# Kernel optimization log

Hardware: AMD Instinct MI355X
Metric: run time of the kernel (lower is better)

Reference implementation:

```python
import jax, jax.numpy as jnp
import numpy as np

W = 32        # local_context
M = 128       # nb_features
TEMP = 1.0    # softmax_temp
NEG = -1e24   # mask fill used by local_dot_product in the original


def _log_features(x, proj):
    # Performer softmax-kernel log-features (before stabilization).
    # x: (B,H,N,E), proj: (M,E) -> (B,H,N,M); exp(q.k*TEMP) ~ (1/M) sum_m phi_q phi_k
    xn = x * np.float32(np.sqrt(TEMP))
    d = jnp.einsum('bhne,me->bhnm', xn, proj)
    diag = 0.5 * jnp.sum(xn * xn, axis=-1, keepdims=True)
    return d - diag


def _sb_local_chunk(q, k, v, proj):
    # Scatterbrain SBLocalAttention: exact softmax scores inside a centered local
    # window of size W, Performer low-rank approximation outside, shared normalizer.
    # q: (B,H,L,E) chunk queries; k,v: (B,H,S,E); proj: (M,E)
    B, H, L, E = q.shape
    S = k.shape[2]
    nb, half = L // W, W // 2

    logq = _log_features(q, proj)
    stab_q = jax.lax.stop_gradient(jnp.max(logq, axis=-1, keepdims=True))        # per-query stabilizer
    phi_q = jnp.exp(logq - stab_q)
    logk = _log_features(k, proj)
    stab_k = jax.lax.stop_gradient(jnp.max(logk, axis=(-1, -2), keepdims=True))  # global key stabilizer
    phi_k = jnp.exp(logk - stab_k)
    # true low-rank score = (phi_q . phi_k) * exp(prime_log_scale)
    pls = stab_q[..., 0] + stab_k[..., 0] - np.float32(np.log(M))                # (B,H,L)

    # Low-rank (linear attention) sums over ALL keys
    kv = jnp.einsum('bhsm,bhsd->bhmd', phi_k, v)
    lr_v = jnp.einsum('bhlm,bhmd->bhld', phi_q, kv)            # (B,H,L,E)
    lr_1 = jnp.einsum('bhlm,bhm->bhl', phi_q, phi_k.sum(2))    # (B,H,L)

    # Local window: query position t attends keys [t-W//2, t+W//2).
    # Gather 3 key blocks of size W per query block instead of per-query windows.
    q_blk = q.reshape(B, H, nb, W, E)
    phiq_blk = phi_q.reshape(B, H, nb, W, M)
    idx3 = W * jnp.arange(nb)[:, None] + jnp.arange(3 * W)[None, :]   # (nb,3W) into padded seq
    pad = [(0, 0), (0, 0), (W, W), (0, 0)]
    k3 = jnp.pad(k, pad)[:, :, idx3]          # (B,H,nb,3W,E)
    v3 = jnp.pad(v, pad)[:, :, idx3]
    phik3 = jnp.pad(phi_k, pad)[:, :, idx3]   # (B,H,nb,3W,M)

    pos = idx3[:, None, :] - W                # absolute key positions (nb,1,3W)
    rel = pos - (W * jnp.arange(nb)[:, None, None] + jnp.arange(W)[None, :, None])
    mask = (rel >= -half) & (rel < half) & (pos >= 0) & (pos < S)     # (nb,W,3W)

    scores = TEMP * jnp.einsum('bhnqe,bhnke->bhnqk', q_blk, k3)
    scores = jnp.where(mask, scores, NEG)
    dots_p = jnp.where(mask, jnp.einsum('bhnqm,bhnkm->bhnqk', phiq_blk, phik3), 0.0)

    qk_lse = jax.nn.logsumexp(scores, axis=-1).reshape(B, H, L)
    # low-rank mass minus the in-window part it double counts (>= 0 since phi >= 0)
    lr_rem = jnp.clip(lr_1 - dots_p.sum(-1).reshape(B, H, L), 1e-24, None)
    log_norm = jnp.logaddexp(qk_lse, jnp.log(lr_rem) + pls)           # (B,H,L)

    p_local = jnp.exp(scores - log_norm.reshape(B, H, nb, W, 1))
    out_local = jnp.einsum('bhnqk,bhnke->bhnqe', p_local, v3).reshape(B, H, L, E)
    lr_v_win = jnp.einsum('bhnqk,bhnke->bhnqe', dots_p, v3).reshape(B, H, L, E)
    return out_local + (lr_v - lr_v_win) * jnp.exp(pls - log_norm)[..., None]


def _forward(query, key, value, proj):
    # query/key/value: (B,T,H,E) as in the torch module; proj: (4,M,E), one random
    # feature matrix per chunk (module builds a fresh SBLocalAttention each chunk).
    q = jnp.transpose(query, (0, 2, 1, 3))
    k = jnp.transpose(key, (0, 2, 1, 3))
    v = jnp.transpose(value, (0, 2, 1, 3))
    B, H, T, E = q.shape
    CH = 1024
    qc = q.reshape(B, H, T // CH, CH, E).transpose(2, 0, 1, 3, 4)     # (4,B,H,CH,E)
    outs = jax.vmap(_sb_local_chunk, in_axes=(0, None, None, 0))(qc, k, v, proj)
    # torch.cat(att, 1).transpose(1, 2) -> (B,H,T,E)
    return outs.transpose(1, 2, 0, 3, 4).reshape(B, H, T, E)


def setup_inputs() -> dict:
    key = jax.random.key(0)
    k1, k2, k3, k4 = jax.random.split(key, 4)
    B, T, S, H, E = 4, 4096, 4096, 8, 64
    return {
        'query': jax.random.normal(k1, (B, T, H, E), dtype=jnp.float32),
        'key': jax.random.normal(k2, (B, S, H, E), dtype=jnp.float32),
        'value': jax.random.normal(k3, (B, S, H, E), dtype=jnp.float32),
        'proj': jax.random.normal(k4, (4, M, E), dtype=jnp.float32),
    }


def reference(query, key, value, proj):
    return _forward(query, key, value, proj)
```

## Files before the change

kernel.cpp:

```cpp
#include <hip/hip_runtime.h>

typedef unsigned short u16;
typedef unsigned int   u32;
typedef __attribute__((ext_vector_type(8))) short short8;
typedef __attribute__((ext_vector_type(4))) float f32x4;

#define LOGM 4.852030263919617f

constexpr int WS_PMAX = 0;
constexpr int WS_K1   = 2048;
constexpr int WS_KV   = 18432;
constexpr int WS_PHIK = 1067008;

__device__ __forceinline__ float b2f(u16 u){ union { u32 i; float f; } x; x.i = ((u32)u) << 16; return x.f; }
__device__ __forceinline__ u16 f2b(float f){ union { float f; u32 i; } x; x.f = f; return (u16)((x.i + 0x7fffu + ((x.i >> 16) & 1u)) >> 16); }

__global__ __launch_bounds__(128) void k_stab(const float* __restrict__ proj,
                                              float* __restrict__ ws){
  __shared__ float red[2];
  const int c = blockIdx.x, tid = threadIdx.x;
  const int wave = tid >> 6, l = tid & 63;
  const float4* pr = (const float4*)(proj + c*8192 + tid*64);
  float pn = 0.f;
  #pragma unroll
  for(int i=0;i<16;i++){ float4 u = pr[i]; pn = fmaf(u.x,u.x,fmaf(u.y,u.y,fmaf(u.z,u.z,fmaf(u.w,u.w,pn)))); }
  #pragma unroll
  for(int o=1;o<64;o<<=1) pn = fmaxf(pn, __shfl_xor(pn, o));
  if(l == 0) red[wave] = pn;
  __syncthreads();
  const float stab = 0.5f * fmaxf(red[0], red[1]);
  if(tid < 32) ws[WS_PMAX + c*32 + tid] = stab;
}

__global__ __launch_bounds__(256, 2) void k_phi(const float* __restrict__ key,
                                                const float* __restrict__ val,
                                                const float* __restrict__ proj,
                                                float* __restrict__ ws){
  __shared__ __align__(16) u16 phit[128*72];
  __shared__ __align__(16) u16 vt[64*72];
  const int tid = threadIdx.x;
  const int wave = tid >> 6, l = tid & 63;
  const int g = l >> 4, r16 = l & 15;
  const int kq = blockIdx.x, combo = blockIdx.y;
  const int c = combo >> 5, b = (combo >> 3) & 3, h = combo & 7;
  const float* projc = proj + c*8192;
  const float stab = ws[WS_PMAX + combo];

  short8 ph[8][2], pl[8][2];
  #pragma unroll
  for(int mt=0;mt<8;mt++){
    #pragma unroll
    for(int ks=0;ks<2;ks++){
      const float* pb = projc + (mt*16 + r16)*64 + ks*32 + g*8;
      float4 u0 = *(const float4*)pb;
      float4 u1 = *(const float4*)(pb + 4);
      float x[8] = {u0.x,u0.y,u0.z,u0.w,u1.x,u1.y,u1.z,u1.w};
      #pragma unroll
      for(int j=0;j<8;j++){
        u16 hb = f2b(x[j]);
        ph[mt][ks][j] = (short)hb;
        pl[mt][ks][j] = (short)f2b(x[j] - b2f(hb));
      }
    }
  }

  const f32x4 zero4 = {0.f,0.f,0.f,0.f};
  f32x4 kvacc[2][4];
  #pragma unroll
  for(int i=0;i<2;i++)
    #pragma unroll
    for(int j=0;j<4;j++) kvacc[i][j] = zero4;
  float k1p0 = 0.f, k1p1 = 0.f;
  u16* phikg = ((u16*)(ws + WS_PHIK)) + (size_t)combo*1056*128;

  for(int t0=0;t0<16;t0++){
    const int s_tile = (kq + 4*t0)*64;
    const bool dtile = (s_tile < 1056);
    const int sA = s_tile + wave*16 + r16;
    const float* krow = key + (size_t)(b*4096 + sA)*512 + h*64;
    float areg[16];
    #pragma unroll
    for(int ks=0;ks<2;ks++){
      float4 u0 = *(const float4*)(krow + ks*32 + g*8);
      float4 u1 = *(const float4*)(krow + ks*32 + g*8 + 4);
      areg[ks*8+0]=u0.x; areg[ks*8+1]=u0.y; areg[ks*8+2]=u0.z; areg[ks*8+3]=u0.w;
      areg[ks*8+4]=u1.x; areg[ks*8+5]=u1.y; areg[ks*8+6]=u1.z; areg[ks*8+7]=u1.w;
    }
    float4 vreg[4];
    #pragma unroll
    for(int i=0;i<4;i++){
      int flat = tid + 256*i;
      int sv = flat >> 4, d4 = (flat & 15)*4;
      vreg[i] = *(const float4*)(val + (size_t)(b*4096 + s_tile + sv)*512 + h*64 + d4);
    }
    float ksq = 0.f;
    #pragma unroll
    for(int e=0;e<16;e++) ksq = fmaf(areg[e], areg[e], ksq);
    ksq += __shfl_xor(ksq, 16);
    ksq += __shfl_xor(ksq, 32);
    ksq *= 0.5f;
    short8 ah[2], al[2];
    #pragma unroll
    for(int ks=0;ks<2;ks++){
      #pragma unroll
      for(int j=0;j<8;j++){
        float x = areg[ks*8+j];
        u16 hb = f2b(x);
        ah[ks][j] = (short)hb;
        al[ks][j] = (short)f2b(x - b2f(hb));
      }
    }
    f32x4 acc[8];
    #pragma unroll
    for(int mt=0;mt<8;mt++) acc[mt] = zero4;
    #pragma unroll
    for(int ks=0;ks<2;ks++){
      #pragma unroll
      for(int mt=0;mt<8;mt++){
        acc[mt] = __builtin_amdgcn_mfma_f32_16x16x32_bf16(ah[ks], ph[mt][ks], acc[mt], 0, 0, 0);
        acc[mt] = __builtin_amdgcn_mfma_f32_16x16x32_bf16(ah[ks], pl[mt][ks], acc[mt], 0, 0, 0);
        acc[mt] = __builtin_amdgcn_mfma_f32_16x16x32_bf16(al[ks], ph[mt][ks], acc[mt], 0, 0, 0);
      }
    }
    const float kc0 = __shfl(ksq, 4*g + 0);
    const float kc1 = __shfl(ksq, 4*g + 1);
    const float kc2 = __shfl(ksq, 4*g + 2);
    const float kc3 = __shfl(ksq, 4*g + 3);
    const int gs = s_tile + wave*16 + r16;
    #pragma unroll
    for(int mt=0;mt<8;mt++){
      ushort4 pw;
      pw.x = f2b(__expf(acc[mt][0] - kc0 - stab));
      pw.y = f2b(__expf(acc[mt][1] - kc1 - stab));
      pw.z = f2b(__expf(acc[mt][2] - kc2 - stab));
      pw.w = f2b(__expf(acc[mt][3] - kc3 - stab));
      *(ushort4*)(phit + (mt*16 + r16)*72 + wave*16 + 4*g) = pw;
      if(dtile && gs < 1056)
        *(ushort4*)(phikg + (size_t)gs*128 + mt*16 + 4*g) = pw;
    }
    #pragma unroll
    for(int i=0;i<4;i++){
      int flat = tid + 256*i;
      int sv = flat >> 4, d4 = (flat & 15)*4;
      float x[4] = {vreg[i].x, vreg[i].y, vreg[i].z, vreg[i].w};
      #pragma unroll
      for(int j=0;j<4;j++){
        int d = d4 + j;
        vt[d*72 + (sv ^ (8*((d>>2)&7)))] = f2b(x[j]);
      }
    }
    __syncthreads();
    #pragma unroll
    for(int ks=0;ks<2;ks++){
      short8 af0 = *(const short8*)(phit + ((2*wave+0)*16 + r16)*72 + ks*32 + g*8);
      short8 af1 = *(const short8*)(phit + ((2*wave+1)*16 + r16)*72 + ks*32 + g*8);
      short8 bf[4];
      #pragma unroll
      for(int dt=0;dt<4;dt++){
        int d = dt*16 + r16;
        int col = (ks*32 + g*8) ^ (8*((d>>2)&7));
        bf[dt] = *(const short8*)(vt + d*72 + col);
      }
      #pragma unroll
      for(int dt=0;dt<4;dt++){
        kvacc[0][dt] = __builtin_amdgcn_mfma_f32_16x16x32_bf16(af0, bf[dt], kvacc[0][dt], 0, 0, 0);
        kvacc[1][dt] = __builtin_amdgcn_mfma_f32_16x16x32_bf16(af1, bf[dt], kvacc[1][dt], 0, 0, 0);
      }
      #pragma unroll
      for(int j=0;j<8;j++){ k1p0 += b2f((u16)af0[j]); k1p1 += b2f((u16)af1[j]); }
    }
    __syncthreads();
  }
  k1p0 += __shfl_xor(k1p0, 16); k1p0 += __shfl_xor(k1p0, 32);
  k1p1 += __shfl_xor(k1p1, 16); k1p1 += __shfl_xor(k1p1, 32);
  if(l < 16){
    atomicAdd(ws + WS_K1 + combo*128 + (2*wave+0)*16 + l, k1p0);
    atomicAdd(ws + WS_K1 + combo*128 + (2*wave+1)*16 + l, k1p1);
  }
  #pragma unroll
  for(int mi=0;mi<2;mi++){
    #pragma unroll
    for(int dt=0;dt<4;dt++){
      #pragma unroll
      for(int rr=0;rr<4;rr++){
        int m = (2*wave+mi)*16 + 4*g + rr;
        int d = dt*16 + r16;
        atomicAdd(ws + WS_KV + (size_t)combo*8192 + m*64 + d, kvacc[mi][dt][rr]);
      }
    }
  }
}

__global__ __launch_bounds__(256, 2) void k_qm(const float* __restrict__ qry,
                                               const float* __restrict__ key,
                                               const float* __restrict__ val,
                                               const float* __restrict__ proj,
                                               float* __restrict__ ws,
                                               float* __restrict__ out){
  __shared__ __align__(16) u16 buf[30720];
  u16* kvtA   = buf;
  u16* phiqsA = buf + 8704;
  float* k1s  = (float*)(buf + 17408);
  u16* khs  = buf;
  u16* kls  = buf + 6912;
  u16* phik = buf + 13824;
  u16* cjh  = buf;
  u16* cjl  = buf + 8704;
  u16* vt   = buf + 17408;
  u16* vtl  = buf + 24064;

  const int tid = threadIdx.x;
  const int wave = tid >> 6, l = tid & 63;
  const int g = l >> 4, r16 = l & 15;
  const int qt = blockIdx.x, combo = blockIdx.y;
  const int c = combo >> 5, b = (combo >> 3) & 3, h = combo & 7;
  const int s_base = qt*64 - 16;
  const float* projc = proj + c*8192;
  const float stab = ws[WS_PMAX + combo];
  const f32x4 zero4 = {0.f,0.f,0.f,0.f};

  if(tid < 128) k1s[tid] = ws[WS_K1 + combo*128 + tid];
  const float* kvg = ws + WS_KV + (size_t)combo*8192;
  #pragma unroll
  for(int i=0;i<8;i++){
    int flat = tid + 256*i;
    int m = flat >> 4, d4 = (flat & 15)*4;
    float4 u = *(const float4*)(kvg + m*64 + d4);
    kvtA[(d4+0)*136 + m] = f2b(u.x);
    kvtA[(d4+1)*136 + m] = f2b(u.y);
    kvtA[(d4+2)*136 + m] = f2b(u.z);
    kvtA[(d4+3)*136 + m] = f2b(u.w);
  }
  const int qrow = qt*64 + wave*16 + r16;
  const float* qr = qry + (size_t)(b*4096 + (c*1024 + qrow))*512 + h*64;
  float areg[16];
  #pragma unroll
  for(int ks=0;ks<2;ks++){
    float4 u0 = *(const float4*)(qr + ks*32 + g*8);
    float4 u1 = *(const float4*)(qr + ks*32 + g*8 + 4);
    areg[ks*8+0]=u0.x; areg[ks*8+1]=u0.y; areg[ks*8+2]=u0.z; areg[ks*8+3]=u0.w;
    areg[ks*8+4]=u1.x; areg[ks*8+5]=u1.y; areg[ks*8+6]=u1.z; areg[ks*8+7]=u1.w;
  }
  float qsq = 0.f;
  #pragma unroll
  for(int e=0;e<16;e++) qsq = fmaf(areg[e], areg[e], qsq);
  qsq += __shfl_xor(qsq, 16);
  qsq += __shfl_xor(qsq, 32);
  qsq *= 0.5f;
  short8 ah[2], al[2];
  #pragma unroll
  for(int ks=0;ks<2;ks++){
    #pragma unroll
    for(int j=0;j<8;j++){
      float x = areg[ks*8+j];
      u16 hb = f2b(x);
      ah[ks][j] = (short)hb;
      al[ks][j] = (short)f2b(x - b2f(hb));
    }
  }
  __syncthreads();

  f32x4 acc[8];
  #pragma unroll
  for(int mt=0;mt<8;mt++) acc[mt] = zero4;
  #pragma unroll
  for(int ks=0;ks<2;ks++){
    #pragma unroll
    for(int mt=0;mt<8;mt++){
      const float* pb = projc + (mt*16 + r16)*64 + ks*32 + g*8;
      float4 u0 = *(const float4*)pb;
      float4 u1 = *(const float4*)(pb + 4);
      float x[8] = {u0.x,u0.y,u0.z,u0.w,u1.x,u1.y,u1.z,u1.w};
      short8 pph, ppl;
      #pragma unroll
      for(int j=0;j<8;j++){
        u16 hb = f2b(x[j]);
        pph[j] = (short)hb;
        ppl[j] = (short)f2b(x[j] - b2f(hb));
      }
      acc[mt] = __builtin_amdgcn_mfma_f32_16x16x32_bf16(ah[ks], pph, acc[mt], 0, 0, 0);
      acc[mt] = __builtin_amdgcn_mfma_f32_16x16x32_bf16(ah[ks], ppl, acc[mt], 0, 0, 0);
      acc[mt] = __builtin_amdgcn_mfma_f32_16x16x32_bf16(al[ks], pph, acc[mt], 0, 0, 0);
    }
  }
  float qsr[4];
  #pragma unroll
  for(int r=0;r<4;r++) qsr[r] = __shfl(qsq, 4*g + r);
  float amax[4];
  #pragma unroll
  for(int r=0;r<4;r++){
    float m = -3e38f;
    #pragma unroll
    for(int mt=0;mt<8;mt++) m = fmaxf(m, acc[mt][r]);
    m = fmaxf(m, __shfl_xor(m, 1));
    m = fmaxf(m, __shfl_xor(m, 2));
    m = fmaxf(m, __shfl_xor(m, 4));
    m = fmaxf(m, __shfl_xor(m, 8));
    amax[r] = m;
  }
  float lrp[4] = {0.f,0.f,0.f,0.f};
  #pragma unroll
  for(int mt=0;mt<8;mt++){
    const float k1v = k1s[mt*16 + r16];
    #pragma unroll
    for(int r=0;r<4;r++){
      float phv = __expf(acc[mt][r] - amax[r]);
      phiqsA[(wave*16 + 4*g + r)*136 + mt*16 + r16] = f2b(phv);
      lrp[r] = fmaf(phv, k1v, lrp[r]);
    }
  }
  #pragma unroll
  for(int r=0;r<4;r++){
    lrp[r] += __shfl_xor(lrp[r], 1);
    lrp[r] += __shfl_xor(lrp[r], 2);
    lrp[r] += __shfl_xor(lrp[r], 4);
    lrp[r] += __shfl_xor(lrp[r], 8);
  }
  float plsr[4], lr1r[4];
  #pragma unroll
  for(int r=0;r<4;r++){
    plsr[r] = amax[r] - qsr[r] + stab - LOGM;
    lr1r[r] = lrp[r];
  }
  __syncthreads();

  short8 pa[4];
  #pragma unroll
  for(int ks=0;ks<4;ks++)
    pa[ks] = *(const short8*)(phiqsA + (wave*16 + r16)*136 + ks*32 + g*8);
  f32x4 lacc[4];
  #pragma unroll
  for(int dt=0;dt<4;dt++) lacc[dt] = zero4;
  #pragma unroll
  for(int ks=0;ks<4;ks++){
    #pragma unroll
    for(int dt=0;dt<4;dt++){
      short8 bfr = *(const short8*)(kvtA + (dt*16 + r16)*136 + ks*32 + g*8);
      lacc[dt] = __builtin_amdgcn_mfma_f32_16x16x32_bf16(pa[ks], bfr, lacc[dt], 0, 0, 0);
    }
  }
  __syncthreads();

  const u16* phikg = ((const u16*)(ws + WS_PHIK)) + (size_t)combo*1056*128;
  float4 vreg[6];
  #pragma unroll
  for(int i=0;i<6;i++){
    int flat = tid + 256*i;
    int j = flat >> 4, e4 = (flat & 15)*4;
    int s = s_base + j;
    float4 u = {0.f,0.f,0.f,0.f};
    float4 w4 = {0.f,0.f,0.f,0.f};
    if(s >= 0){
      u  = *(const float4*)(key + (((size_t)b*4096 + s)*8 + h)*64 + e4);
      w4 = *(const float4*)(val + (((size_t)b*4096 + s)*8 + h)*64 + e4);
    }
    vreg[i] = w4;
    ushort4 hh, ll;
    hh.x = f2b(u.x); ll.x = f2b(u.x - b2f(hh.x));
    hh.y = f2b(u.y); ll.y = f2b(u.y - b2f(hh.y));
    hh.z = f2b(u.z); ll.z = f2b(u.z - b2f(hh.z));
    hh.w = f2b(u.w); ll.w = f2b(u.w - b2f(hh.w));
    *(ushort4*)(khs + j*72 + e4) = hh;
    *(ushort4*)(kls + j*72 + e4) = ll;
  }
  #pragma unroll
  for(int i=0;i<12;i++){
    int flat = tid + 256*i;
    int j = flat >> 5, c4 = (flat & 31)*4;
    int s = s_base + j;
    ushort4 p = {0,0,0,0};
    if(s >= 0) p = *(const ushort4*)(phikg + (size_t)s*128 + c4);
    *(ushort4*)(phik + j*136 + c4) = p;
  }
  __syncthreads();

  f32x4 sacc[6], dacc[6];
  #pragma unroll
  for(int j=0;j<6;j++){ sacc[j] = zero4; dacc[j] = zero4; }
  #pragma unroll
  for(int j=0;j<6;j++){
    #pragma unroll
    for(int ks=0;ks<2;ks++){
      short8 kbh = *(const short8*)(khs + (j*16 + r16)*72 + ks*32 + g*8);
      short8 kbl = *(const short8*)(kls + (j*16 + r16)*72 + ks*32 + g*8);
      sacc[j] = __builtin_amdgcn_mfma_f32_16x16x32_bf16(ah[ks], kbh, sacc[j], 0, 0, 0);
      sacc[j] = __builtin_amdgcn_mfma_f32_16x16x32_bf16(al[ks], kbh, sacc[j], 0, 0, 0);
      sacc[j] = __builtin_amdgcn_mfma_f32_16x16x32_bf16(ah[ks], kbl, sacc[j], 0, 0, 0);
    }
    #pragma unroll
    for(int ks=0;ks<4;ks++){
      short8 pb = *(const short8*)(phik + (j*16 + r16)*136 + ks*32 + g*8);
      dacc[j] = __builtin_amdgcn_mfma_f32_16x16x32_bf16(pa[ks], pb, dacc[j], 0, 0, 0);
    }
  }
  __syncthreads();

  #pragma unroll
  for(int i=0;i<6;i++){
    int flat = tid + 256*i;
    int j = flat >> 4, e4 = (flat & 15)*4;
    float4 u = vreg[i];
    u16 h0 = f2b(u.x), h1 = f2b(u.y), h2 = f2b(u.z), h3 = f2b(u.w);
    vt[(e4+0)*104 + j] = h0; vtl[(e4+0)*104 + j] = f2b(u.x - b2f(h0));
    vt[(e4+1)*104 + j] = h1; vtl[(e4+1)*104 + j] = f2b(u.y - b2f(h1));
    vt[(e4+2)*104 + j] = h2; vtl[(e4+2)*104 + j] = f2b(u.z - b2f(h2));
    vt[(e4+3)*104 + j] = h3; vtl[(e4+3)*104 + j] = f2b(u.w - b2f(h3));
  }
  const int rowb = wave*16 + 4*g;
  float m1r[4] = {-1e30f,-1e30f,-1e30f,-1e30f};
  #pragma unroll
  for(int j=0;j<6;j++){
    #pragma unroll
    for(int r=0;r<4;r++){
      int rel = 16*j + r16 - 16 - (rowb + r);
      bool ok = (rel >= -16) && (rel < 16) && (s_base + 16*j + r16 >= 0);
      if(ok) m1r[r] = fmaxf(m1r[r], sacc[j][r]);
    }
  }
  #pragma unroll
  for(int r=0;r<4;r++){
    m1r[r] = fmaxf(m1r[r], __shfl_xor(m1r[r], 1));
    m1r[r] = fmaxf(m1r[r], __shfl_xor(m1r[r], 2));
    m1r[r] = fmaxf(m1r[r], __shfl_xor(m1r[r], 4));
    m1r[r] = fmaxf(m1r[r], __shfl_xor(m1r[r], 8));
  }
  float ser[4] = {0.f,0.f,0.f,0.f}, wpr[4] = {0.f,0.f,0.f,0.f};
  #pragma unroll
  for(int j=0;j<6;j++){
    #pragma unroll
    for(int r=0;r<4;r++){
      int rel = 16*j + r16 - 16 - (rowb + r);
      bool ok = (rel >= -16) && (rel < 16) && (s_base + 16*j + r16 >= 0);
      if(ok){
        ser[r] += __expf(sacc[j][r] - m1r[r]);
        wpr[r] += dacc[j][r];
      }
    }
  }
  #pragma unroll
  for(int r=0;r<4;r++){
    ser[r] += __shfl_xor(ser[r], 1); ser[r] += __shfl_xor(ser[r], 2);
    ser[r] += __shfl_xor(ser[r], 4); ser[r] += __shfl_xor(ser[r], 8);
    wpr[r] += __shfl_xor(wpr[r], 1); wpr[r] += __shfl_xor(wpr[r], 2);
    wpr[r] += __shfl_xor(wpr[r], 4); wpr[r] += __shfl_xor(wpr[r], 8);
  }
  float lnr[4], scr[4];
  #pragma unroll
  for(int r=0;r<4;r++){
    float qk_lse = m1r[r] + __logf(ser[r]);
    float lrem = fmaxf(lr1r[r] - wpr[r], 1e-37f);
    float bb = __logf(lrem) + plsr[r];
    float ln = fmaxf(qk_lse, bb) + log1pf(__expf(-fabsf(qk_lse - bb)));
    lnr[r] = ln;
    scr[r] = __expf(plsr[r] - ln);
  }
  #pragma unroll
  for(int j=0;j<6;j++){
    #pragma unroll
    for(int r=0;r<4;r++){
      int rel = 16*j + r16 - 16 - (rowb + r);
      bool ok = (rel >= -16) && (rel < 16) && (s_base + 16*j + r16 >= 0);
      float cj = ok ? (__expf(sacc[j][r] - lnr[r]) - scr[r]*dacc[j][r]) : 0.f;
      u16 hb = f2b(cj);
      cjh[(rowb + r)*136 + 16*j + r16] = hb;
      cjl[(rowb + r)*136 + 16*j + r16] = f2b(cj - b2f(hb));
    }
  }
  __syncthreads();

  f32x4 oacc[4];
  #pragma unroll
  for(int dt=0;dt<4;dt++) oacc[dt] = zero4;
  #pragma unroll
  for(int ks=0;ks<3;ks++){
    short8 ch = *(const short8*)(cjh + (wave*16 + r16)*136 + ks*32 + g*8);
    short8 cl = *(const short8*)(cjl + (wave*16 + r16)*136 + ks*32 + g*8);
    #pragma unroll
    for(int dt=0;dt<4;dt++){
      short8 vbh = *(const short8*)(vt  + (dt*16 + r16)*104 + ks*32 + g*8);
      short8 vbl = *(const short8*)(vtl + (dt*16 + r16)*104 + ks*32 + g*8);
      oacc[dt] = __builtin_amdgcn_mfma_f32_16x16x32_bf16(ch, vbh, oacc[dt], 0, 0, 0);
      oacc[dt] = __builtin_amdgcn_mfma_f32_16x16x32_bf16(cl, vbh, oacc[dt], 0, 0, 0);
      oacc[dt] = __builtin_amdgcn_mfma_f32_16x16x32_bf16(ch, vbl, oacc[dt], 0, 0, 0);
    }
  }
  #pragma unroll
  for(int r=0;r<4;r++){
    int row = rowb + r;
    float* ob = out + ((((size_t)b*8 + h)*4096) + (size_t)c*1024 + qt*64 + row)*64;
    #pragma unroll
    for(int dt=0;dt<4;dt++)
      ob[dt*16 + r16] = oacc[dt][r] + scr[r]*lacc[dt][r];
  }
}

extern "C" void kernel_launch(void* const* d_in, const int* in_sizes, int n_in,
                              void* d_out, int out_size, void* d_ws, size_t ws_size,
                              hipStream_t stream){
  (void)in_sizes; (void)n_in; (void)out_size; (void)ws_size;
  const float* q = (const float*)d_in[0];
  const float* k = (const float*)d_in[1];
  const float* v = (const float*)d_in[2];
  const float* p = (const float*)d_in[3];
  float* out = (float*)d_out;
  float* ws = (float*)d_ws;
  hipMemsetAsync(ws + WS_K1, 0, (size_t)(16384 + 1048576)*sizeof(float), stream);
  k_stab<<<dim3(4),      128, 0, stream>>>(p, ws);
  k_phi <<<dim3(4,128),  256, 0, stream>>>(k, v, p, ws);
  k_qm  <<<dim3(16,128), 256, 0, stream>>>(q, k, v, p, ws, out);
}
```

Baseline: 324.1 us.

## Prefetch key/value/phi_k tiles early and XOR-swizzle LDS transposed buffers

Moves the global loads of the key, value and phi_k window tiles to the start of the main kernel, holding them in registers so their latency overlaps the query feature and low-rank MFMA phases. It also applies XOR swizzles to the column index of the transposed kv, v and cj shared-memory buffers to reduce LDS bank conflicts on the strided transpose stores. The prefetch adds about 48 live registers per thread, which may lower occupancy or cause spills.

Result: faster. 315.9 us (-2.5%).

```diff
diff --git a/kernel.cpp b/kernel.cpp
--- a/kernel.cpp
+++ b/kernel.cpp
@@ -219,130 +219,9 @@
   const float stab = ws[WS_PMAX + combo];
   const f32x4 zero4 = {0.f,0.f,0.f,0.f};
 
-  if(tid < 128) k1s[tid] = ws[WS_K1 + combo*128 + tid];
-  const float* kvg = ws + WS_KV + (size_t)combo*8192;
-  #pragma unroll
-  for(int i=0;i<8;i++){
-    int flat = tid + 256*i;
-    int m = flat >> 4, d4 = (flat & 15)*4;
-    float4 u = *(const float4*)(kvg + m*64 + d4);
-    kvtA[(d4+0)*136 + m] = f2b(u.x);
-    kvtA[(d4+1)*136 + m] = f2b(u.y);
-    kvtA[(d4+2)*136 + m] = f2b(u.z);
-    kvtA[(d4+3)*136 + m] = f2b(u.w);
-  }
-  const int qrow = qt*64 + wave*16 + r16;
-  const float* qr = qry + (size_t)(b*4096 + (c*1024 + qrow))*512 + h*64;
-  float areg[16];
-  #pragma unroll
-  for(int ks=0;ks<2;ks++){
-    float4 u0 = *(const float4*)(qr + ks*32 + g*8);
-    float4 u1 = *(const float4*)(qr + ks*32 + g*8 + 4);
-    areg[ks*8+0]=u0.x; areg[ks*8+1]=u0.y; areg[ks*8+2]=u0.z; areg[ks*8+3]=u0.w;
-    areg[ks*8+4]=u1.x; areg[ks*8+5]=u1.y; areg[ks*8+6]=u1.z; areg[ks*8+7]=u1.w;
-  }
-  float qsq = 0.f;
-  #pragma unroll
-  for(int e=0;e<16;e++) qsq = fmaf(areg[e], areg[e], qsq);
-  qsq += __shfl_xor(qsq, 16);
-  qsq += __shfl_xor(qsq, 32);
-  qsq *= 0.5f;
-  short8 ah[2], al[2];
-  #pragma unroll
-  for(int ks=0;ks<2;ks++){
-    #pragma unroll
-    for(int j=0;j<8;j++){
-      float x = areg[ks*8+j];
-      u16 hb = f2b(x);
-      ah[ks][j] = (short)hb;
-      al[ks][j] = (short)f2b(x - b2f(hb));
-    }
-  }
-  __syncthreads();
-
-  f32x4 acc[8];
-  #pragma unroll
-  for(int mt=0;mt<8;mt++) acc[mt] = zero4;
-  #pragma unroll
-  for(int ks=0;ks<2;ks++){
-    #pragma unroll
-    for(int mt=0;mt<8;mt++){
-      const float* pb = projc + (mt*16 + r16)*64 + ks*32 + g*8;
-      float4 u0 = *(const float4*)pb;
-      float4 u1 = *(const float4*)(pb + 4);
-      float x[8] = {u0.x,u0.y,u0.z,u0.w,u1.x,u1.y,u1.z,u1.w};
-      short8 pph, ppl;
-      #pragma unroll
-      for(int j=0;j<8;j++){
-        u16 hb = f2b(x[j]);
-        pph[j] = (short)hb;
-        ppl[j] = (short)f2b(x[j] - b2f(hb));
-      }
-      acc[mt] = __builtin_amdgcn_mfma_f32_16x16x32_bf16(ah[ks], pph, acc[mt], 0, 0, 0);
-      acc[mt] = __builtin_amdgcn_mfma_f32_16x16x32_bf16(ah[ks], ppl, acc[mt], 0, 0, 0);
-      acc[mt] = __builtin_amdgcn_mfma_f32_16x16x32_bf16(al[ks], pph, acc[mt], 0, 0, 0);
-    }
-  }
-  float qsr[4];
-  #pragma unroll
-  for(int r=0;r<4;r++) qsr[r] = __shfl(qsq, 4*g + r);
-  float amax[4];
-  #pragma unroll
-  for(int r=0;r<4;r++){
-    float m = -3e38f;
-    #pragma unroll
-    for(int mt=0;mt<8;mt++) m = fmaxf(m, acc[mt][r]);
-    m = fmaxf(m, __shfl_xor(m, 1));
-    m = fmaxf(m, __shfl_xor(m, 2));
-    m = fmaxf(m, __shfl_xor(m, 4));
-    m = fmaxf(m, __shfl_xor(m, 8));
-    amax[r] = m;
-  }
-  float lrp[4] = {0.f,0.f,0.f,0.f};
-  #pragma unroll
-  for(int mt=0;mt<8;mt++){
-    const float k1v = k1s[mt*16 + r16];
-    #pragma unroll
-    for(int r=0;r<4;r++){
-      float phv = __expf(acc[mt][r] - amax[r]);
-      phiqsA[(wave*16 + 4*g + r)*136 + mt*16 + r16] = f2b(phv);
-      lrp[r] = fmaf(phv, k1v, lrp[r]);
-    }
-  }
-  #pragma unroll
-  for(int r=0;r<4;r++){
-    lrp[r] += __shfl_xor(lrp[r], 1);
-    lrp[r] += __shfl_xor(lrp[r], 2);
-    lrp[r] += __shfl_xor(lrp[r], 4);
-    lrp[r] += __shfl_xor(lrp[r], 8);
-  }
-  float plsr[4], lr1r[4];
-  #pragma unroll
-  for(int r=0;r<4;r++){
-    plsr[r] = amax[r] - qsr[r] + stab - LOGM;
-    lr1r[r] = lrp[r];
-  }
-  __syncthreads();
-
-  short8 pa[4];
-  #pragma unroll
-  for(int ks=0;ks<4;ks++)
-    pa[ks] = *(const short8*)(phiqsA + (wave*16 + r16)*136 + ks*32 + g*8);
-  f32x4 lacc[4];
-  #pragma unroll
-  for(int dt=0;dt<4;dt++) lacc[dt] = zero4;
-  #pragma unroll
-  for(int ks=0;ks<4;ks++){
-    #pragma unroll
-    for(int dt=0;dt<4;dt++){
-      short8 bfr = *(const short8*)(kvtA + (dt*16 + r16)*136 + ks*32 + g*8);
-      lacc[dt] = __builtin_amdgcn_mfma_f32_16x16x32_bf16(pa[ks], bfr, lacc[dt], 0, 0, 0);
-    }
-  }
-  __syncthreads();
-
   const u16* phikg = ((const u16*)(ws + WS_PHIK)) + (size_t)combo*1056*128;
-  float4 vreg[6];
+  float4 kreg[6], vreg[6];
+  ushort4 preg[12];
   #pragma unroll
   for(int i=0;i<6;i++){
     int flat = tid + 256*i;
@@ -354,7 +233,148 @@
       u  = *(const float4*)(key + (((size_t)b*4096 + s)*8 + h)*64 + e4);
       w4 = *(const float4*)(val + (((size_t)b*4096 + s)*8 + h)*64 + e4);
     }
-    vreg[i] = w4;
+    kreg[i] = u; vreg[i] = w4;
+  }
+  #pragma unroll
+  for(int i=0;i<12;i++){
+    int flat = tid + 256*i;
+    int j = flat >> 5, c4 = (flat & 31)*4;
+    int s = s_base + j;
+    ushort4 p = {0,0,0,0};
+    if(s >= 0) p = *(const ushort4*)(phikg + (size_t)s*128 + c4);
+    preg[i] = p;
+  }
+
+  if(tid < 128) k1s[tid] = ws[WS_K1 + combo*128 + tid];
+  const float* kvg = ws + WS_KV + (size_t)combo*8192;
+  #pragma unroll
+  for(int i=0;i<8;i++){
+    int flat = tid + 256*i;
+    int m = flat >> 4, d4 = (flat & 15)*4;
+    int col = m ^ (8*((flat & 15) & 7));
+    float4 u = *(const float4*)(kvg + m*64 + d4);
+    kvtA[(d4+0)*136 + col] = f2b(u.x);
+    kvtA[(d4+1)*136 + col] = f2b(u.y);
+    kvtA[(d4+2)*136 + col] = f2b(u.z);
+    kvtA[(d4+3)*136 + col] = f2b(u.w);
+  }
+  const int qrow = qt*64 + wave*16 + r16;
+  const float* qr = qry + (size_t)(b*4096 + (c*1024 + qrow))*512 + h*64;
+  float areg[16];
+  #pragma unroll
+  for(int ks=0;ks<2;ks++){
+    float4 u0 = *(const float4*)(qr + ks*32 + g*8);
+    float4 u1 = *(const float4*)(qr + ks*32 + g*8 + 4);
+    areg[ks*8+0]=u0.x; areg[ks*8+1]=u0.y; areg[ks*8+2]=u0.z; areg[ks*8+3]=u0.w;
+    areg[ks*8+4]=u1.x; areg[ks*8+5]=u1.y; areg[ks*8+6]=u1.z; areg[ks*8+7]=u1.w;
+  }
+  float qsq = 0.f;
+  #pragma unroll
+  for(int e=0;e<16;e++) qsq = fmaf(areg[e], areg[e], qsq);
+  qsq += __shfl_xor(qsq, 16);
+  qsq += __shfl_xor(qsq, 32);
+  qsq *= 0.5f;
+  short8 ah[2], al[2];
+  #pragma unroll
+  for(int ks=0;ks<2;ks++){
+    #pragma unroll
+    for(int j=0;j<8;j++){
+      float x = areg[ks*8+j];
+      u16 hb = f2b(x);
+      ah[ks][j] = (short)hb;
+      al[ks][j] = (short)f2b(x - b2f(hb));
+    }
+  }
+  __syncthreads();
+
+  f32x4 acc[8];
+  #pragma unroll
+  for(int mt=0;mt<8;mt++) acc[mt] = zero4;
+  #pragma unroll
+  for(int ks=0;ks<2;ks++){
+    #pragma unroll
+    for(int mt=0;mt<8;mt++){
+      const float* pb = projc + (mt*16 + r16)*64 + ks*32 + g*8;
+      float4 u0 = *(const float4*)pb;
+      float4 u1 = *(const float4*)(pb + 4);
+      float x[8] = {u0.x,u0.y,u0.z,u0.w,u1.x,u1.y,u1.z,u1.w};
+      short8 pph, ppl;
+      #pragma unroll
+      for(int j=0;j<8;j++){
+        u16 hb = f2b(x[j]);
+        pph[j] = (short)hb;
+        ppl[j] = (short)f2b(x[j] - b2f(hb));
+      }
+      acc[mt] = __builtin_amdgcn_mfma_f32_16x16x32_bf16(ah[ks], pph, acc[mt], 0, 0, 0);
+      acc[mt] = __builtin_amdgcn_mfma_f32_16x16x32_bf16(ah[ks], ppl, acc[mt], 0, 0, 0);
+      acc[mt] = __builtin_amdgcn_mfma_f32_16x16x32_bf16(al[ks], pph, acc[mt], 0, 0, 0);
+    }
+  }
+  float qsr[4];
+  #pragma unroll
+  for(int r=0;r<4;r++) qsr[r] = __shfl(qsq, 4*g + r);
+  float amax[4];
+  #pragma unroll
+  for(int r=0;r<4;r++){
+    float m = -3e38f;
+    #pragma unroll
+    for(int mt=0;mt<8;mt++) m = fmaxf(m, acc[mt][r]);
+    m = fmaxf(m, __shfl_xor(m, 1));
+    m = fmaxf(m, __shfl_xor(m, 2));
+    m = fmaxf(m, __shfl_xor(m, 4));
+    m = fmaxf(m, __shfl_xor(m, 8));
+    amax[r] = m;
+  }
+  float lrp[4] = {0.f,0.f,0.f,0.f};
+  #pragma unroll
+  for(int mt=0;mt<8;mt++){
+    const float k1v = k1s[mt*16 + r16];
+    #pragma unroll
+    for(int r=0;r<4;r++){
+      float phv = __expf(acc[mt][r] - amax[r]);
+      phiqsA[(wave*16 + 4*g + r)*136 + mt*16 + r16] = f2b(phv);
+      lrp[r] = fmaf(phv, k1v, lrp[r]);
+    }
+  }
+  #pragma unroll
+  for(int r=0;r<4;r++){
+    lrp[r] += __shfl_xor(lrp[r], 1);
+    lrp[r] += __shfl_xor(lrp[r], 2);
+    lrp[r] += __shfl_xor(lrp[r], 4);
+    lrp[r] += __shfl_xor(lrp[r], 8);
+  }
+  float plsr[4], lr1r[4];
+  #pragma unroll
+  for(int r=0;r<4;r++){
+    plsr[r] = amax[r] - qsr[r] + stab - LOGM;
+    lr1r[r] = lrp[r];
+  }
+  __syncthreads();
+
+  short8 pa[4];
+  #pragma unroll
+  for(int ks=0;ks<4;ks++)
+    pa[ks] = *(const short8*)(phiqsA + (wave*16 + r16)*136 + ks*32 + g*8);
+  f32x4 lacc[4];
+  #pragma unroll
+  for(int dt=0;dt<4;dt++) lacc[dt] = zero4;
+  #pragma unroll
+  for(int ks=0;ks<4;ks++){
+    #pragma unroll
+    for(int dt=0;dt<4;dt++){
+      int drow = dt*16 + r16;
+      int colb = (ks*32 + g*8) ^ (8*((drow>>2)&7));
+      short8 bfr = *(const short8*)(kvtA + drow*136 + colb);
+      lacc[dt] = __builtin_amdgcn_mfma_f32_16x16x32_bf16(pa[ks], bfr, lacc[dt], 0, 0, 0);
+    }
+  }
+  __syncthreads();
+
+  #pragma unroll
+  for(int i=0;i<6;i++){
+    int flat = tid + 256*i;
+    int j = flat >> 4, e4 = (flat & 15)*4;
+    float4 u = kreg[i];
     ushort4 hh, ll;
     hh.x = f2b(u.x); ll.x = f2b(u.x - b2f(hh.x));
     hh.y = f2b(u.y); ll.y = f2b(u.y - b2f(hh.y));
@@ -367,10 +387,7 @@
   for(int i=0;i<12;i++){
     int flat = tid + 256*i;
     int j = flat >> 5, c4 = (flat & 31)*4;
-    int s = s_base + j;
-    ushort4 p = {0,0,0,0};
-    if(s >= 0) p = *(const ushort4*)(phikg + (size_t)s*128 + c4);
-    *(ushort4*)(phik + j*136 + c4) = p;
+    *(ushort4*)(phik + j*136 + c4) = preg[i];
   }
   __syncthreads();
 
@@ -399,12 +416,14 @@
   for(int i=0;i<6;i++){
     int flat = tid + 256*i;
     int j = flat >> 4, e4 = (flat & 15)*4;
+    int e = flat & 15;
+    int col = j ^ (8*(e & 3));
     float4 u = vreg[i];
     u16 h0 = f2b(u.x), h1 = f2b(u.y), h2 = f2b(u.z), h3 = f2b(u.w);
-    vt[(e4+0)*104 + j] = h0; vtl[(e4+0)*104 + j] = f2b(u.x - b2f(h0));
-    vt[(e4+1)*104 + j] = h1; vtl[(e4+1)*104 + j] = f2b(u.y - b2f(h1));
-    vt[(e4+2)*104 + j] = h2; vtl[(e4+2)*104 + j] = f2b(u.z - b2f(h2));
-    vt[(e4+3)*104 + j] = h3; vtl[(e4+3)*104 + j] = f2b(u.w - b2f(h3));
+    vt[(e4+0)*104 + col] = h0; vtl[(e4+0)*104 + col] = f2b(u.x - b2f(h0));
+    vt[(e4+1)*104 + col] = h1; vtl[(e4+1)*104 + col] = f2b(u.y - b2f(h1));
+    vt[(e4+2)*104 + col] = h2; vtl[(e4+2)*104 + col] = f2b(u.z - b2f(h2));
+    vt[(e4+3)*104 + col] = h3; vtl[(e4+3)*104 + col] = f2b(u.w - b2f(h3));
   }
   const int rowb = wave*16 + 4*g;
   float m1r[4] = {-1e30f,-1e30f,-1e30f,-1e30f};
@@ -462,8 +481,10 @@
       bool ok = (rel >= -16) && (rel < 16) && (s_base + 16*j + r16 >= 0);
       float cj = ok ? (__expf(sacc[j][r] - lnr[r]) - scr[r]*dacc[j][r]) : 0.f;
       u16 hb = f2b(cj);
-      cjh[(rowb + r)*136 + 16*j + r16] = hb;
-      cjl[(rowb + r)*136 + 16*j + r16] = f2b(cj - b2f(hb));
+      int row = rowb + r;
+      int col = (16*j + r16) ^ (8*((row>>2)&7));
+      cjh[row*136 + col] = hb;
+      cjl[row*136 + col] = f2b(cj - b2f(hb));
     }
   }
   __syncthreads();
@@ -471,14 +492,19 @@
   f32x4 oacc[4];
   #pragma unroll
   for(int dt=0;dt<4;dt++) oacc[dt] = zero4;
+  const int qrowB = wave*16 + r16;
+  const int cw = (qrowB >> 2) & 7;
   #pragma unroll
   for(int ks=0;ks<3;ks++){
-    short8 ch = *(const short8*)(cjh + (wave*16 + r16)*136 + ks*32 + g*8);
-    short8 cl = *(const short8*)(cjl + (wave*16 + r16)*136 + ks*32 + g*8);
+    int ccol = (ks*32 + g*8) ^ (8*cw);
+    short8 ch = *(const short8*)(cjh + qrowB*136 + ccol);
+    short8 cl = *(const short8*)(cjl + qrowB*136 + ccol);
     #pragma unroll
     for(int dt=0;dt<4;dt++){
-      short8 vbh = *(const short8*)(vt  + (dt*16 + r16)*104 + ks*32 + g*8);
-      short8 vbl = *(const short8*)(vtl + (dt*16 + r16)*104 + ks*32 + g*8);
+      int vrow = dt*16 + r16;
+      int vcol = (ks*32 + g*8) ^ (8*((vrow>>2)&3));
+      short8 vbh = *(const short8*)(vt  + vrow*104 + vcol);
+      short8 vbl = *(const short8*)(vtl + vrow*104 + vcol);
       oacc[dt] = __builtin_amdgcn_mfma_f32_16x16x32_bf16(ch, vbh, oacc[dt], 0, 0, 0);
       oacc[dt] = __builtin_amdgcn_mfma_f32_16x16x32_bf16(cl, vbh, oacc[dt], 0, 0, 0);
       oacc[dt] = __builtin_amdgcn_mfma_f32_16x16x32_bf16(ch, vbl, oacc[dt], 0, 0, 0);
```
